# Kernel tuning notes

Measured on AMD Instinct MI355X. Metric: run time of the kernel, lower is better.

The kernel has to match this reference:

```python
import jax, jax.numpy as jnp
import numpy as np

N_NODES = 50000
N_EDGES = 800000
D_IN, D_HID, D_LAT = 128, 128, 64
BN_EPS = 1e-5


def setup_inputs() -> dict:
    key = jax.random.key(0)
    ks = jax.random.split(key, 8)
    x = jax.random.normal(ks[0], (N_NODES, D_IN), dtype=jnp.float32)
    edge_index = jax.random.randint(ks[1], (2, N_EDGES), 0, N_NODES, dtype=jnp.int64)
    s1 = 1.0 / np.sqrt(D_IN)
    s2 = 1.0 / np.sqrt(D_HID)
    W1 = jax.random.normal(ks[2], (D_IN, D_HID), dtype=jnp.float32) * s1
    b1 = jnp.zeros((D_HID,), jnp.float32)
    gamma = jnp.ones((D_HID,), jnp.float32)
    beta = jnp.zeros((D_HID,), jnp.float32)
    Wmu = jax.random.normal(ks[3], (D_HID, D_LAT), dtype=jnp.float32) * s2
    bmu = jnp.zeros((D_LAT,), jnp.float32)
    Wls = jax.random.normal(ks[4], (D_HID, D_LAT), dtype=jnp.float32) * s2
    bls = jnp.zeros((D_LAT,), jnp.float32)
    return {"x": x, "edge_index": edge_index, "W1": W1, "b1": b1,
            "gamma": gamma, "beta": beta, "Wmu": Wmu, "bmu": bmu,
            "Wls": Wls, "bls": bls}


def _gcn_conv(h, src, dst, norm_e, inv_deg, W, b):
    # PyG GCNConv: linear transform, then sym-normalized aggregation (A+I).
    h = h @ W                                   # [N, F]
    msgs = h[src] * norm_e[:, None]             # gather + edge scaling, [E, F]
    agg = jax.ops.segment_sum(msgs, dst, num_segments=h.shape[0])
    # self-loop contribution: norm[i]*norm[i] = 1/deg[i]
    return agg + h * inv_deg[:, None] + b


def reference(x, edge_index, W1, b1, gamma, beta, Wmu, bmu, Wls, bls):
    src, dst = edge_index[0], edge_index[1]
    n = x.shape[0]
    # degrees including self loops (GCN symmetric normalization)
    deg = jax.ops.segment_sum(jnp.ones(dst.shape, x.dtype), dst, num_segments=n) + 1.0
    inv_sqrt_deg = jax.lax.rsqrt(deg)
    norm_e = inv_sqrt_deg[src] * inv_sqrt_deg[dst]   # per-edge norm, [E]
    inv_deg = 1.0 / deg

    h = _gcn_conv(x, src, dst, norm_e, inv_deg, W1, b1)
    # BatchNorm1d with batch statistics (biased var), then ReLU; dropout off (eval)
    mean = h.mean(axis=0)
    var = h.var(axis=0)
    h = (h - mean) * jax.lax.rsqrt(var + BN_EPS) * gamma + beta
    h = jax.nn.relu(h)

    mu = _gcn_conv(h, src, dst, norm_e, inv_deg, Wmu, bmu)
    log_std = _gcn_conv(h, src, dst, norm_e, inv_deg, Wls, bls)
    return mu, log_std
```

## Files before the change

### kernel.cpp

```cpp
#include <hip/hip_runtime.h>
#include <hip/hip_bf16.h>

#define N_NODES 50000
#define N_EDGES 800000
#define F 128
#define L 64
#define BN_EPS 1e-5f
#define SCAN_BLOCKS 196
#define BN_BLOCKS 391

typedef __attribute__((ext_vector_type(8))) short short8;
typedef __attribute__((ext_vector_type(8))) unsigned short ushort8;
typedef __attribute__((ext_vector_type(4))) float f32x4;

static __device__ __forceinline__ float loadF(const void* p, int i, int f32) {
    if (f32) return ((const float*)p)[i];
    return __bfloat162float(((const __hip_bfloat16*)p)[i]);
}
static __device__ __forceinline__ int loadI(const void* p, int i, int i64) {
    if (i64) return (int)((const long long*)p)[i];
    return ((const int*)p)[i];
}
static __device__ __forceinline__ float bfu2f(unsigned short u) {
    unsigned int t = ((unsigned int)u) << 16;
    float f;
    __builtin_memcpy(&f, &t, 4);
    return f;
}
static __device__ __forceinline__ short f2bf_s(float f) {
    union { __hip_bfloat16 b; short s; } cv;
    cv.b = __float2bfloat16(f);
    return cv.s;
}
static __device__ __forceinline__ unsigned short f2bf_u(float f) {
    union { __hip_bfloat16 b; unsigned short u; } cv;
    cv.b = __float2bfloat16(f);
    return cv.u;
}

__global__ void k_detect(const unsigned short* xs, const int* ei, int* flags) {
    __shared__ int cnt[2];
    if (threadIdx.x < 2) cnt[threadIdx.x] = 0;
    __syncthreads();
    int t = threadIdx.x;
    unsigned short v = xs[2 * t];
    int e = (v >> 7) & 0xff;
    int sane = (e >= 112 && e <= 133) ? 1 : 0;
    if (v == 0 || v == 0x8000) sane = 1;
    atomicAdd(&cnt[0], sane);
    atomicAdd(&cnt[1], (ei[2 * t + 1] != 0) ? 1 : 0);
    __syncthreads();
    if (threadIdx.x == 0) {
        flags[0] = (cnt[0] < 128) ? 1 : 0;
        flags[1] = (cnt[1] < 8) ? 1 : 0;
    }
}

__global__ void k_deg(const void* ei, const int* __restrict__ flags, int* __restrict__ degi) {
    int e = blockIdx.x * blockDim.x + threadIdx.x;
    if (e < N_EDGES) atomicAdd(&degi[loadI(ei, N_EDGES + e, flags[1])], 1);
}

__global__ void k_bsum(const int* __restrict__ degi, int* __restrict__ bsum) {
    int i = blockIdx.x * 256 + threadIdx.x;
    int v = (i < N_NODES) ? degi[i] : 0;
#pragma unroll
    for (int o = 32; o; o >>= 1) v += __shfl_down(v, o);
    __shared__ int ws[4];
    if ((threadIdx.x & 63) == 0) ws[threadIdx.x >> 6] = v;
    __syncthreads();
    if (threadIdx.x == 0) bsum[blockIdx.x] = ws[0] + ws[1] + ws[2] + ws[3];
}

__global__ void k_scanb(const int* __restrict__ bsum, int* __restrict__ boff,
                        int* __restrict__ offs) {
    __shared__ int s[256];
    int t = threadIdx.x;
    int v = (t < SCAN_BLOCKS) ? bsum[t] : 0;
    s[t] = v;
    __syncthreads();
    for (int o = 1; o < 256; o <<= 1) {
        int u = (t >= o) ? s[t - o] : 0;
        __syncthreads();
        s[t] += u;
        __syncthreads();
    }
    boff[t] = s[t] - v;
    if (t == 0) offs[N_NODES] = N_EDGES;
}

__global__ void k_offs(int* __restrict__ degi, const int* __restrict__ boff,
                       int* __restrict__ offs, float* __restrict__ isd) {
    __shared__ int s[256];
    int i = blockIdx.x * 256 + threadIdx.x;
    int t = threadIdx.x;
    int v = (i < N_NODES) ? degi[i] : 0;
    s[t] = v;
    __syncthreads();
    for (int o = 1; o < 256; o <<= 1) {
        int u = (t >= o) ? s[t - o] : 0;
        __syncthreads();
        s[t] += u;
        __syncthreads();
    }
    if (i < N_NODES) {
        offs[i] = boff[blockIdx.x] + s[t] - v;
        isd[i] = 1.0f / sqrtf((float)v + 1.0f);
        degi[i] = 0;
    }
}

__global__ void k_fill(const void* ei, const int* __restrict__ flags,
                       const int* __restrict__ offs, int* __restrict__ cur,
                       int* __restrict__ csr) {
    int e = blockIdx.x * blockDim.x + threadIdx.x;
    if (e < N_EDGES) {
        int i64 = flags[1];
        int s = loadI(ei, e, i64);
        int d = loadI(ei, N_EDGES + e, i64);
        int pos = offs[d] + atomicAdd(&cur[d], 1);
        csr[pos] = s;
    }
}

__global__ void k_prepW(const void* __restrict__ W1, const void* __restrict__ Wmu,
                        const void* __restrict__ Wls, const int* __restrict__ flags,
                        __hip_bfloat16* __restrict__ Wt1, __hip_bfloat16* __restrict__ Wt2) {
    int idx = blockIdx.x * 256 + threadIdx.x;
    int n = idx >> 7, k = idx & 127;
    int f32 = flags[0];
    Wt1[idx] = __float2bfloat16(loadF(W1, k * F + n, f32));
    float v2 = (n < L) ? loadF(Wmu, k * L + n, f32) : loadF(Wls, k * L + (n - L), f32);
    Wt2[idx] = __float2bfloat16(v2);
}

__global__ __launch_bounds__(256) void k_gemm_mfma(const void* __restrict__ Xin,
        const __hip_bfloat16* __restrict__ Wt, const float* __restrict__ isd,
        const int* __restrict__ flags, int mode,
        const float* __restrict__ bnscale, const float* __restrict__ bnshift,
        unsigned short* __restrict__ outb) {
    int wave = threadIdx.x >> 6, lane = threadIdx.x & 63;
    int quad = lane >> 4, mr = lane & 15;
    int m0 = blockIdx.x * 64 + wave * 16;
    int row = m0 + mr;
    if (row >= N_NODES) row = N_NODES - 1;
    short8 a[4];
    if (mode == 1) {
        const unsigned short* xb = (const unsigned short*)Xin;
#pragma unroll
        for (int t = 0; t < 4; ++t) {
            int k0 = t * 32 + quad * 8;
            ushort8 raw = *(const ushort8*)(xb + row * F + k0);
            short8 av;
#pragma unroll
            for (int j = 0; j < 8; ++j) {
                float v = bfu2f(raw[j]) * bnscale[k0 + j] + bnshift[k0 + j];
                av[j] = f2bf_s(fmaxf(v, 0.f));
            }
            a[t] = av;
        }
    } else if (flags[0]) {
        const float* xf = (const float*)Xin;
#pragma unroll
        for (int t = 0; t < 4; ++t) {
            int off = row * F + t * 32 + quad * 8;
            short8 av;
#pragma unroll
            for (int j = 0; j < 8; ++j) av[j] = f2bf_s(xf[off + j]);
            a[t] = av;
        }
    } else {
        const short* xb = (const short*)Xin;
#pragma unroll
        for (int t = 0; t < 4; ++t)
            a[t] = *(const short8*)(xb + row * F + t * 32 + quad * 8);
    }
    f32x4 acc[8];
    const short* wb = (const short*)Wt;
#pragma unroll
    for (int nt = 0; nt < 8; ++nt) {
        const short* wp = wb + (nt * 16 + mr) * F + quad * 8;
        f32x4 c = {0.f, 0.f, 0.f, 0.f};
        c = __builtin_amdgcn_mfma_f32_16x16x32_bf16(a[0], *(const short8*)(wp), c, 0, 0, 0);
        c = __builtin_amdgcn_mfma_f32_16x16x32_bf16(a[1], *(const short8*)(wp + 32), c, 0, 0, 0);
        c = __builtin_amdgcn_mfma_f32_16x16x32_bf16(a[2], *(const short8*)(wp + 64), c, 0, 0, 0);
        c = __builtin_amdgcn_mfma_f32_16x16x32_bf16(a[3], *(const short8*)(wp + 96), c, 0, 0, 0);
        acc[nt] = c;
    }
    float sd[4];
    int orow[4];
#pragma unroll
    for (int r = 0; r < 4; ++r) {
        orow[r] = m0 + quad * 4 + r;
        sd[r] = (orow[r] < N_NODES) ? isd[orow[r]] : 0.f;
    }
#pragma unroll
    for (int nt = 0; nt < 8; ++nt)
#pragma unroll
        for (int r = 0; r < 4; ++r)
            if (orow[r] < N_NODES)
                outb[orow[r] * F + nt * 16 + mr] = f2bf_u(acc[nt][r] * sd[r]);
}

__global__ void k_agg1(const unsigned short* __restrict__ val, const int* __restrict__ csr,
                       const int* __restrict__ offs, const float* __restrict__ isd,
                       const void* __restrict__ b1, const int* __restrict__ flags,
                       unsigned short* __restrict__ out) {
    int node = blockIdx.x * 4 + (threadIdx.x >> 6);
    if (node >= N_NODES) return;
    int lane = threadIdx.x & 63;
    int grp = lane >> 4, l16 = lane & 15;
    const ushort8* vp = (const ushort8*)val;
    float acc[8] = {0.f, 0.f, 0.f, 0.f, 0.f, 0.f, 0.f, 0.f};
    if (grp == 0) {
        ushort8 u = vp[node * 16 + l16];
#pragma unroll
        for (int j = 0; j < 8; ++j) acc[j] = bfu2f(u[j]);
    }
    int end = offs[node + 1];
    int i = offs[node] + grp;
    for (; i + 4 < end; i += 8) {
        ushort8 u0 = vp[csr[i] * 16 + l16];
        ushort8 u1 = vp[csr[i + 4] * 16 + l16];
#pragma unroll
        for (int j = 0; j < 8; ++j) acc[j] += bfu2f(u0[j]) + bfu2f(u1[j]);
    }
    for (; i < end; i += 4) {
        ushort8 u = vp[csr[i] * 16 + l16];
#pragma unroll
        for (int j = 0; j < 8; ++j) acc[j] += bfu2f(u[j]);
    }
#pragma unroll
    for (int j = 0; j < 8; ++j) {
        acc[j] += __shfl_xor(acc[j], 16);
        acc[j] += __shfl_xor(acc[j], 32);
    }
    if (grp == 0) {
        float sd = isd[node];
        int c0 = l16 * 8, f32 = flags[0];
        ushort8 r;
#pragma unroll
        for (int j = 0; j < 8; ++j) r[j] = f2bf_u(acc[j] * sd + loadF(b1, c0 + j, f32));
        ((ushort8*)out)[node * 16 + l16] = r;
    }
}

__global__ void k_bnstats(const unsigned short* __restrict__ h, float* __restrict__ partial) {
    __shared__ float ls[256][8];
    __shared__ float lq[256][8];
    int t = threadIdx.x;
    int o = t & 15, rg = t >> 4;
    int row0 = blockIdx.x * 128 + rg;
    float s[8] = {0.f}, q[8] = {0.f};
#pragma unroll
    for (int i = 0; i < 8; ++i) {
        int row = row0 + i * 16;
        if (row < N_NODES) {
            ushort8 u = *(const ushort8*)(h + row * F + o * 8);
#pragma unroll
            for (int j = 0; j < 8; ++j) {
                float v = bfu2f(u[j]);
                s[j] += v;
                q[j] += v * v;
            }
        }
    }
#pragma unroll
    for (int j = 0; j < 8; ++j) { ls[t][j] = s[j]; lq[t][j] = q[j]; }
    __syncthreads();
    if (t < 128) {
        int c = t, oo = c >> 3, jj = c & 7;
        float ts = 0.f, tq = 0.f;
#pragma unroll
        for (int rgi = 0; rgi < 16; ++rgi) {
            ts += ls[rgi * 16 + oo][jj];
            tq += lq[rgi * 16 + oo][jj];
        }
        partial[blockIdx.x * 256 + c] = ts;
        partial[blockIdx.x * 256 + 128 + c] = tq;
    }
}

__global__ void k_bnred(const float* __restrict__ partial, float* __restrict__ stats) {
    int j = blockIdx.x;
    float a = 0.f;
    for (int b = threadIdx.x; b < BN_BLOCKS; b += 256) a += partial[b * 256 + j];
#pragma unroll
    for (int o = 32; o; o >>= 1) a += __shfl_down(a, o);
    __shared__ float ws[4];
    if ((threadIdx.x & 63) == 0) ws[threadIdx.x >> 6] = a;
    __syncthreads();
    if (threadIdx.x == 0) stats[j] = ws[0] + ws[1] + ws[2] + ws[3];
}

__global__ void k_bnprep(const float* __restrict__ sum, const float* __restrict__ sumsq,
                         const void* __restrict__ gamma, const void* __restrict__ beta,
                         const int* __restrict__ flags, float* __restrict__ scale,
                         float* __restrict__ shift) {
    int c = threadIdx.x;
    int f32 = flags[0];
    const float invN = 1.0f / (float)N_NODES;
    float m = sum[c] * invN;
    float var = sumsq[c] * invN - m * m;
    float sc = loadF(gamma, c, f32) * rsqrtf(var + BN_EPS);
    scale[c] = sc;
    shift[c] = loadF(beta, c, f32) - m * sc;
}

__global__ void k_agg2(const unsigned short* __restrict__ val, const int* __restrict__ csr,
                       const int* __restrict__ offs, const float* __restrict__ isd,
                       const void* __restrict__ bmu, const void* __restrict__ bls,
                       const int* __restrict__ flags, void* __restrict__ out) {
    int node = blockIdx.x * 4 + (threadIdx.x >> 6);
    if (node >= N_NODES) return;
    int lane = threadIdx.x & 63;
    int grp = lane >> 4, l16 = lane & 15;
    const ushort8* vp = (const ushort8*)val;
    float acc[8] = {0.f, 0.f, 0.f, 0.f, 0.f, 0.f, 0.f, 0.f};
    if (grp == 0) {
        ushort8 u = vp[node * 16 + l16];
#pragma unroll
        for (int j = 0; j < 8; ++j) acc[j] = bfu2f(u[j]);
    }
    int end = offs[node + 1];
    int i = offs[node] + grp;
    for (; i + 4 < end; i += 8) {
        ushort8 u0 = vp[csr[i] * 16 + l16];
        ushort8 u1 = vp[csr[i + 4] * 16 + l16];
#pragma unroll
        for (int j = 0; j < 8; ++j) acc[j] += bfu2f(u0[j]) + bfu2f(u1[j]);
    }
    for (; i < end; i += 4) {
        ushort8 u = vp[csr[i] * 16 + l16];
#pragma unroll
        for (int j = 0; j < 8; ++j) acc[j] += bfu2f(u[j]);
    }
#pragma unroll
    for (int j = 0; j < 8; ++j) {
        acc[j] += __shfl_xor(acc[j], 16);
        acc[j] += __shfl_xor(acc[j], 32);
    }
    if (grp == 0) {
        float sd = isd[node];
        int c0 = l16 * 8, f32 = flags[0];
        int hsel = (c0 >= L) ? 1 : 0;
        int cc = c0 - hsel * L;
        const void* bp = hsel ? bls : bmu;
        float o8[8];
#pragma unroll
        for (int j = 0; j < 8; ++j) o8[j] = acc[j] * sd + loadF(bp, cc + j, f32);
        long base_o = (long)hsel * (N_NODES * 64) + (long)node * 64 + cc;
        if (f32) {
            float4 r0 = make_float4(o8[0], o8[1], o8[2], o8[3]);
            float4 r1 = make_float4(o8[4], o8[5], o8[6], o8[7]);
            *(float4*)((float*)out + base_o) = r0;
            *(float4*)((float*)out + base_o + 4) = r1;
        } else {
            ushort8 r;
#pragma unroll
            for (int j = 0; j < 8; ++j) r[j] = f2bf_u(o8[j]);
            *(ushort8*)((__hip_bfloat16*)out + base_o) = r;
        }
    }
}

extern "C" void kernel_launch(void* const* d_in, const int* in_sizes, int n_in,
                              void* d_out, int out_size, void* d_ws, size_t ws_size,
                              hipStream_t stream) {
    const void* x     = d_in[0];
    const void* ei    = d_in[1];
    const void* W1    = d_in[2];
    const void* b1    = d_in[3];
    const void* gamma = d_in[4];
    const void* beta  = d_in[5];
    const void* Wmu   = d_in[6];
    const void* bmu   = d_in[7];
    const void* Wls   = d_in[8];
    const void* bls   = d_in[9];

    int*   degi  = (int*)d_ws;
    int*   offs  = degi + 50048;
    float* isd   = (float*)(offs + 50048);
    float* stats = isd + 50000;
    int*   flags = (int*)(stats + 512);
    int*   bsum  = flags + 16;
    int*   boff  = bsum + 256;
    int*   csr   = boff + 256;
    __hip_bfloat16* Wt1 = (__hip_bfloat16*)(csr + 800000);
    __hip_bfloat16* Wt2 = Wt1 + 16384;
    unsigned short* Abf = (unsigned short*)(Wt2 + 16384);
    unsigned short* Hpre = Abf + N_NODES * F;
    float* partial = (float*)(Hpre + N_NODES * F);

    hipMemsetAsync(degi, 0, N_NODES * sizeof(int), stream);

    const int NT = 256;
    const int AGG_BLOCKS = (N_NODES + 3) / 4;
    const int GEMM_BLOCKS = (N_NODES + 63) / 64;

    k_detect<<<1, NT, 0, stream>>>((const unsigned short*)x, (const int*)ei, flags);
    k_prepW<<<64, NT, 0, stream>>>(W1, Wmu, Wls, flags, Wt1, Wt2);
    k_deg<<<(N_EDGES + NT - 1) / NT, NT, 0, stream>>>(ei, flags, degi);
    k_bsum<<<SCAN_BLOCKS, NT, 0, stream>>>(degi, bsum);
    k_scanb<<<1, NT, 0, stream>>>(bsum, boff, offs);
    k_offs<<<SCAN_BLOCKS, NT, 0, stream>>>(degi, boff, offs, isd);
    k_fill<<<(N_EDGES + NT - 1) / NT, NT, 0, stream>>>(ei, flags, offs, degi, csr);

    k_gemm_mfma<<<GEMM_BLOCKS, NT, 0, stream>>>(x, Wt1, isd, flags, 0, nullptr, nullptr, Abf);
    k_agg1<<<AGG_BLOCKS, NT, 0, stream>>>(Abf, csr, offs, isd, b1, flags, Hpre);

    k_bnstats<<<BN_BLOCKS, NT, 0, stream>>>(Hpre, partial);
    k_bnred<<<256, NT, 0, stream>>>(partial, stats);
    k_bnprep<<<1, 128, 0, stream>>>(stats, stats + 128, gamma, beta, flags,
                                    stats + 256, stats + 384);

    k_gemm_mfma<<<GEMM_BLOCKS, NT, 0, stream>>>(Hpre, Wt2, isd, flags, 1,
                                                stats + 256, stats + 384, Abf);
    k_agg2<<<AGG_BLOCKS, NT, 0, stream>>>(Abf, csr, offs, isd, bmu, bls, flags, d_out);
}
```

Measured before the change: 330.3 us.

## Convert edge indices to int32 once and partition CSR fill by destination range

The degree kernel now also writes int32 copies of the source and destination indices, so the CSR fill reads compact arrays instead of int64 edge_index again. The fill kernel is restructured so each of 8 block groups scans all edges but only handles destinations in its own node range. The aim is locality for the atomics and scattered csr writes, giving better cache hit rates. The cost is that every group rereads the full dst array (8x reads), which adds traffic and may outweigh the locality gain.

```diff
diff --git a/kernel.cpp b/kernel.cpp
--- a/kernel.cpp
+++ b/kernel.cpp
@@ -8,6 +8,8 @@
 #define BN_EPS 1e-5f
 #define SCAN_BLOCKS 196
 #define BN_BLOCKS 391
+#define NPART 8
+#define PART_SZ 6250
 
 typedef __attribute__((ext_vector_type(8))) short short8;
 typedef __attribute__((ext_vector_type(8))) unsigned short ushort8;
@@ -56,9 +58,18 @@
     }
 }
 
-__global__ void k_deg(const void* ei, const int* __restrict__ flags, int* __restrict__ degi) {
+__global__ void k_eiprep(const void* ei, const int* __restrict__ flags,
+                         int* __restrict__ src32, int* __restrict__ dst32,
+                         int* __restrict__ degi) {
     int e = blockIdx.x * blockDim.x + threadIdx.x;
-    if (e < N_EDGES) atomicAdd(&degi[loadI(ei, N_EDGES + e, flags[1])], 1);
+    if (e < N_EDGES) {
+        int i64 = flags[1];
+        int s = loadI(ei, e, i64);
+        int d = loadI(ei, N_EDGES + e, i64);
+        src32[e] = s;
+        dst32[e] = d;
+        atomicAdd(&degi[d], 1);
+    }
 }
 
 __global__ void k_bsum(const int* __restrict__ degi, int* __restrict__ bsum) {
@@ -110,16 +121,19 @@
     }
 }
 
-__global__ void k_fill(const void* ei, const int* __restrict__ flags,
+__global__ void k_fill(const int* __restrict__ src32, const int* __restrict__ dst32,
                        const int* __restrict__ offs, int* __restrict__ cur,
                        int* __restrict__ csr) {
-    int e = blockIdx.x * blockDim.x + threadIdx.x;
-    if (e < N_EDGES) {
-        int i64 = flags[1];
-        int s = loadI(ei, e, i64);
-        int d = loadI(ei, N_EDGES + e, i64);
-        int pos = offs[d] + atomicAdd(&cur[d], 1);
-        csr[pos] = s;
+    int grp = blockIdx.x & (NPART - 1);
+    int sub = blockIdx.x >> 3;
+    int lo = grp * PART_SZ, hi = lo + PART_SZ;
+    int stride = (gridDim.x >> 3) * blockDim.x;
+    for (int e = sub * blockDim.x + threadIdx.x; e < N_EDGES; e += stride) {
+        int d = dst32[e];
+        if (d >= lo && d < hi) {
+            int pos = offs[d] + atomicAdd(&cur[d], 1);
+            csr[pos] = src32[e];
+        }
     }
 }
 
@@ -386,7 +400,9 @@
     int*   bsum  = flags + 16;
     int*   boff  = bsum + 256;
     int*   csr   = boff + 256;
-    __hip_bfloat16* Wt1 = (__hip_bfloat16*)(csr + 800000);
+    int*   src32 = csr + 800000;
+    int*   dst32 = src32 + 800000;
+    __hip_bfloat16* Wt1 = (__hip_bfloat16*)(dst32 + 800000);
     __hip_bfloat16* Wt2 = Wt1 + 16384;
     unsigned short* Abf = (unsigned short*)(Wt2 + 16384);
     unsigned short* Hpre = Abf + N_NODES * F;
@@ -400,11 +416,11 @@
 
     k_detect<<<1, NT, 0, stream>>>((const unsigned short*)x, (const int*)ei, flags);
     k_prepW<<<64, NT, 0, stream>>>(W1, Wmu, Wls, flags, Wt1, Wt2);
-    k_deg<<<(N_EDGES + NT - 1) / NT, NT, 0, stream>>>(ei, flags, degi);
+    k_eiprep<<<(N_EDGES + NT - 1) / NT, NT, 0, stream>>>(ei, flags, src32, dst32, degi);
     k_bsum<<<SCAN_BLOCKS, NT, 0, stream>>>(degi, bsum);
     k_scanb<<<1, NT, 0, stream>>>(bsum, boff, offs);
     k_offs<<<SCAN_BLOCKS, NT, 0, stream>>>(degi, boff, offs, isd);
-    k_fill<<<(N_EDGES + NT - 1) / NT, NT, 0, stream>>>(ei, flags, offs, degi, csr);
+    k_fill<<<512, NT, 0, stream>>>(src32, dst32, offs, degi, csr);
 
     k_gemm_mfma<<<GEMM_BLOCKS, NT, 0, stream>>>(x, Wt1, isd, flags, 0, nullptr, nullptr, Abf);
     k_agg1<<<AGG_BLOCKS, NT, 0, stream>>>(Abf, csr, offs, isd, b1, flags, Hpre);
```

Result: no change. 328.3 us (-0.6%).
